# Performance work log

Hardware: AMD Instinct MI355X
Metric: run time of the kernel (lower is better)

## Reference

```python
import jax, jax.numpy as jnp
import numpy as np

M = 64    # multiplicity (channels per harmonic degree)
P = 64    # positional encoding dim
EPS = 1e-5


def sinusoidal_pe(N, P):
    pos = jnp.arange(N, dtype=jnp.float32)[:, None]
    div = jnp.exp(jnp.arange(0, P, 2, dtype=jnp.float32) * (-np.log(10000.0) / P))
    pe = jnp.zeros((N, P), dtype=jnp.float32)
    pe = pe.at[:, 0::2].set(jnp.sin(pos * div))
    pe = pe.at[:, 1::2].set(jnp.cos(pos * div))
    return pe


def split_irreps(h):
    # h: [B, N, 4M] -> scalar part [B,N,M], vector part [B,N,M,3]
    B, N, _ = h.shape
    h4 = h.reshape(B, N, M, 4)
    return h4[..., 0], h4[..., 1:]


def merge_irreps(s, v):
    B, N, _ = s.shape
    return jnp.concatenate([s[..., None], v], axis=-1).reshape(B, N, M * 4)


def hyena_block(h, Wq, Wk, Wv, filt, Wo):
    # Hyena-style gated long convolution: q * conv(k * v), FFT circular conv along seq
    N = h.shape[1]
    q = h @ Wq
    k = h @ Wk
    v = h @ Wv
    kf = jnp.fft.rfft(filt, n=N, axis=0)                       # [N//2+1, H]
    conv = jnp.fft.irfft(jnp.fft.rfft(k * v, n=N, axis=1) * kf[None], n=N, axis=1)
    return (q * conv) @ Wo


def reg_linear(h, W0, W1):
    # degree-wise linear mixing across multiplicity (equivariant)
    s, v = split_irreps(h)
    return merge_irreps(jnp.einsum('bnm,mk->bnk', s, W0),
                        jnp.einsum('bnmd,mk->bnkd', v, W1))


def reg_batchnorm(h, g0, g1):
    # normalize per-channel irrep norms over (batch, tokens); learnable per-channel gain
    s, v = split_irreps(h)
    n0 = jnp.sqrt(jnp.mean(s * s, axis=(0, 1)) + EPS)          # [M]
    n1 = jnp.sqrt(jnp.mean(jnp.sum(v * v, axis=-1), axis=(0, 1)) + EPS)
    return merge_irreps(s / n0 * g0, v / n1[:, None] * g1[:, None])


def norm_activation(h):
    # norm-gated nonlinearity: each irrep scaled by sigmoid of its norm (equivariant)
    s, v = split_irreps(h)
    vn = jnp.sqrt(jnp.sum(v * v, axis=-1, keepdims=True) + EPS)
    return merge_irreps(s * jax.nn.sigmoid(jnp.abs(s)), v * jax.nn.sigmoid(vn))


def setup_inputs() -> dict:
    key = jax.random.key(0)
    B, N = 64, 1024
    D = M * 4
    H = [360, 360, 160]   # 10*sum(2l+1,l<=5)=360, 360, 10*sum(2l+1,l<=3)=160
    ks = iter(jax.random.split(key, 64))
    def rn(shape, scale=0.02):
        return jax.random.normal(next(ks), shape, dtype=jnp.float32) * scale
    inp = {
        'x': jax.random.normal(next(ks), (B, N, 3), dtype=jnp.float32),
        'tok_emb': rn((3, P)),
        'Wf': rn((P, M)),
        'wv': rn((M,), 0.5),
        'w_out': rn((M,), 0.5),
    }
    for i, Hi in enumerate(H, start=1):
        inp[f'Wq{i}'] = rn((D, Hi)); inp[f'Wk{i}'] = rn((D, Hi)); inp[f'Wv{i}'] = rn((D, Hi))
        inp[f'filt{i}'] = rn((N, Hi)); inp[f'Wo{i}'] = rn((Hi, D))
        inp[f'Wm0_{i}'] = rn((M, M)); inp[f'Wm1_{i}'] = rn((M, M))
        inp[f'g0_{i}'] = jnp.ones((M,), jnp.float32); inp[f'g1_{i}'] = jnp.ones((M,), jnp.float32)
    return inp


def reference(x, tok_emb, Wf, wv, w_out,
              Wq1, Wk1, Wv1, filt1, Wo1, Wm0_1, Wm1_1, g0_1, g1_1,
              Wq2, Wk2, Wv2, filt2, Wo2, Wm0_2, Wm1_2, g0_2, g1_2,
              Wq3, Wk3, Wv3, filt3, Wo3, Wm0_3, Wm1_3, g0_3, g1_3):
    B, N, _ = x.shape
    # invariant features: sinusoidal PE + token-type embedding (alternating 0/1, last token 2)
    pe = sinusoidal_pe(N, P)
    tt = jnp.arange(N) % 2
    tt = tt.at[-1].set(2)
    f = pe + tok_emb[tt]                                        # [N, P]
    # input conversion: invariants -> degree-0 channels; input vector -> degree-1 channels
    s0 = jnp.broadcast_to((f @ Wf)[None], (B, N, M))
    v0 = x[:, :, None, :] * wv[None, None, :, None]             # [B, N, M, 3]
    h = merge_irreps(s0, v0)                                    # [B, N, 4M]
    layers = [
        (Wq1, Wk1, Wv1, filt1, Wo1, Wm0_1, Wm1_1, g0_1, g1_1),
        (Wq2, Wk2, Wv2, filt2, Wo2, Wm0_2, Wm1_2, g0_2, g1_2),
        (Wq3, Wk3, Wv3, filt3, Wo3, Wm0_3, Wm1_3, g0_3, g1_3),
    ]
    for (Wq, Wk, Wv_, filt, Wo, Wm0, Wm1, g0, g1) in layers:
        h = h + hyena_block(h, Wq, Wk, Wv_, filt, Wo)           # hyena + residual
        y = reg_linear(h, Wm0, Wm1)                             # mlp
        y = reg_batchnorm(y, g0, g1)                            # batch norm
        y = norm_activation(y)                                  # norm activation
        h = h + y                                               # residual
    pooled = h.mean(axis=1)                                     # [B, 4M] mean pool over tokens
    _, vpool = split_irreps(pooled[:, None, :])                 # [B, 1, M, 3]
    return jnp.einsum('bmd,m->bd', vpool[:, 0], w_out)          # [B, 3]
```

## Files before the change

### kernel.cpp

```cpp
#include <hip/hip_runtime.h>
#include <math.h>

namespace {

typedef __bf16 bf16_t;
typedef bf16_t bf16x8 __attribute__((ext_vector_type(8)));
typedef float floatx4 __attribute__((ext_vector_type(4)));

constexpr int kN = 1024;
constexpr int kM = 64;
constexpr int kP = 64;
constexpr float kEps = 1e-5f;
constexpr int kFN = 1024;
constexpr size_t kYOFF = 16777216;

__device__ __forceinline__ float sigmoidf(float v) { return 1.0f / (1.0f + expf(-v)); }

__device__ __forceinline__ floatx4 mfma16(bf16x8 a, bf16x8 b, floatx4 c) {
  return __builtin_amdgcn_mfma_f32_16x16x32_bf16(a, b, c, 0, 0, 0);
}

__device__ __forceinline__ void fma3(floatx4& acc, bf16x8 ah, bf16x8 al,
                                     bf16x8 bh, bf16x8 bl) {
  acc = mfma16(ah, bh, acc);
  acc = mfma16(ah, bl, acc);
  acc = mfma16(al, bh, acc);
}

__device__ __forceinline__ void fma2(floatx4& acc, bf16x8 ah, bf16x8 bh, bf16x8 bl) {
  acc = mfma16(ah, bh, acc);
  acc = mfma16(ah, bl, acc);
}

union U4 { uint4 u; bf16_t b[8]; };
union Pk4 { uint2 u; bf16_t b[4]; };
union Ub2 { uint u; bf16_t b[2]; };

__device__ __forceinline__ void glds16(const bf16_t* g, bf16_t* l) {
  __builtin_amdgcn_global_load_lds(
      (const __attribute__((address_space(1))) void*)g,
      (__attribute__((address_space(3))) void*)l, 16, 0, 0);
}

__device__ __forceinline__ size_t hidx(int r, int d8) {
  const int rb = r >> 6, rr = r & 63;
  return (size_t)(rb * 8 + (d8 >> 2)) * 4096 + (rr >> 4) * 1024 + (d8 & 3) * 128 + (rr & 15) * 8;
}

__device__ __forceinline__ int zi(int i) { return i + (i >> 4); }

__device__ __forceinline__ float2 cadd(float2 a, float2 b) { return {a.x + b.x, a.y + b.y}; }
__device__ __forceinline__ float2 csub(float2 a, float2 b) { return {a.x - b.x, a.y - b.y}; }
__device__ __forceinline__ float2 cmul(float2 a, float2 w) {
  return {a.x * w.x - a.y * w.y, a.x * w.y + a.y * w.x};
}
__device__ __forceinline__ float2 cmulc(float2 a, float2 w) {
  return {a.x * w.x + a.y * w.y, a.y * w.x - a.x * w.y};
}

__global__ void k_s0(const float* __restrict__ tok_emb, const float* __restrict__ Wf,
                     float* __restrict__ s0) {
  __shared__ float f[kP];
  const int n = blockIdx.x;
  const int t = threadIdx.x;
  const int tt = (n == kN - 1) ? 2 : (n & 1);
  const int j = t >> 1;
  const float cexp = (float)(-9.210340371976184 / 64.0);
  const float divj = expf((float)(2 * j) * cexp);
  const float ang = (float)n * divj;
  const float pe = (t & 1) ? cosf(ang) : sinf(ang);
  f[t] = pe + tok_emb[tt * kP + t];
  __syncthreads();
  float acc = 0.0f;
#pragma unroll 8
  for (int p = 0; p < kP; ++p) acc = fmaf(f[p], Wf[p * kM + t], acc);
  s0[n * kM + t] = acc;
}

__global__ void k_h0(const float* __restrict__ x, const float* __restrict__ wv,
                     const float* __restrict__ s0, bf16_t* __restrict__ hsh) {
  const int idx = blockIdx.x * 256 + threadIdx.x;
  const int r = idx >> 5, d8 = idx & 31;
  const int n = r & (kN - 1);
  const int m0 = d8 * 2, m1 = m0 + 1;
  const float w0 = wv[m0], w1 = wv[m1];
  const float x0 = x[r * 3 + 0], x1 = x[r * 3 + 1], x2 = x[r * 3 + 2];
  float f[8];
  f[0] = s0[n * kM + m0]; f[1] = x0 * w0; f[2] = x1 * w0; f[3] = x2 * w0;
  f[4] = s0[n * kM + m1]; f[5] = x0 * w1; f[6] = x1 * w1; f[7] = x2 * w1;
  U4 oh, ol;
#pragma unroll
  for (int i = 0; i < 8; ++i) {
    const bf16_t h_ = (bf16_t)f[i];
    oh.b[i] = h_; ol.b[i] = (bf16_t)(f[i] - (float)h_);
  }
  const size_t base = hidx(r, d8);
  *(uint4*)(hsh + base) = oh.u;
  *(uint4*)(hsh + base + 512) = ol.u;
}

__global__ void k_wqkv3(const float* __restrict__ Wq0, const float* __restrict__ Wk0,
                        const float* __restrict__ Wv0,
                        const float* __restrict__ Wq1, const float* __restrict__ Wk1,
                        const float* __restrict__ Wv1,
                        const float* __restrict__ Wq2, const float* __restrict__ Wk2,
                        const float* __restrict__ Wv2, bf16_t* __restrict__ wall3) {
  const int l = blockIdx.y;
  const int H = (l == 2) ? 160 : 360;
  const int gy = (l == 2) ? 3 : 6;
  const int c = blockIdx.x;
  if (c >= gy * 64) return;
  const int k = threadIdx.x;
  const float* Wq = (l == 0) ? Wq0 : ((l == 1) ? Wq1 : Wq2);
  const float* Wk = (l == 0) ? Wk0 : ((l == 1) ? Wk1 : Wk2);
  const float* Wv = (l == 0) ? Wv0 : ((l == 1) ? Wv1 : Wv2);
  bf16_t* wall = wall3 + ((l == 2) ? 1179648 : (size_t)l * 589824);
  const bool ok = c < H;
  const float w[3] = {ok ? Wq[k * H + c] : 0.f, ok ? Wk[k * H + c] : 0.f,
                      ok ? Wv[k * H + c] : 0.f};
  const int ct = c >> 6, cgrp = (c >> 4) & 3, cl = c & 15;
  const int kc = k >> 5, quad = (k >> 3) & 3, off = k & 7;
  const size_t base = (size_t)(ct * 8 + kc) * 12288 + cgrp * 512 + quad * 128 + cl * 8 + off;
#pragma unroll
  for (int mat = 0; mat < 3; ++mat) {
    const bf16_t hi = (bf16_t)w[mat];
    wall[base + mat * 4096] = hi;
    wall[base + mat * 4096 + 2048] = (bf16_t)(w[mat] - (float)hi);
  }
}

__global__ void k_wo3(const float* __restrict__ Wo0, const float* __restrict__ Wo1,
                      const float* __restrict__ Wo2, bf16_t* __restrict__ WoF3) {
  const int l = blockIdx.y;
  const int H = (l == 2) ? 160 : 360;
  const float* Wo = (l == 0) ? Wo0 : ((l == 1) ? Wo1 : Wo2);
  bf16_t* WoF = WoF3 + (size_t)l * 196608;
  const int d = blockIdx.x;
  const int c = threadIdx.x;
  const float w = (c < H) ? Wo[c * 256 + d] : 0.f;
  const int dt = d >> 6, dgrp = (d >> 4) & 3, dl = d & 15;
  const int kc = c >> 5, quad = (c >> 3) & 3, off = c & 7;
  const size_t base = (size_t)(dt * 12 + kc) * 4096 + dgrp * 512 + quad * 128 + dl * 8 + off;
  const bf16_t hi = (bf16_t)w;
  WoF[base] = hi;
  WoF[base + 2048] = (bf16_t)(w - (float)hi);
}

__global__ void k_bt3(const float* __restrict__ W00, const float* __restrict__ W10,
                      const float* __restrict__ W01, const float* __restrict__ W11,
                      const float* __restrict__ W02, const float* __restrict__ W12,
                      bf16_t* __restrict__ BtF3) {
  const int l = blockIdx.y;
  const float* W0 = (l == 0) ? W00 : ((l == 1) ? W01 : W02);
  const float* W1 = (l == 0) ? W10 : ((l == 1) ? W11 : W12);
  bf16_t* BtF = BtF3 + (size_t)l * 131072;
  const int col = blockIdx.x, row = threadIdx.x;
  const int k = col >> 2, ck = col & 3, m = row >> 2, cm = row & 3;
  float v = 0.f;
  if (cm == ck) v = (ck == 0 ? W0 : W1)[m * 64 + k];
  const int ct = col >> 6, cgrp = (col >> 4) & 3, cl = col & 15;
  const int kc = row >> 5, quad = (row >> 3) & 3, off = row & 7;
  const size_t base = (size_t)(ct * 8 + kc) * 4096 + cgrp * 512 + quad * 128 + cl * 8 + off;
  const bf16_t hi = (bf16_t)v;
  BtF[base] = hi;
  BtF[base + 2048] = (bf16_t)(v - (float)hi);
}

__global__ void k_tw(float2* __restrict__ twg) {
  const int j = blockIdx.x * 256 + threadIdx.x;
  if (j < kFN / 2) {
    float s, c;
    sincosf(-6.283185307179586f * (float)j / (float)kFN, &s, &c);
    twg[j].x = c; twg[j].y = s;
  }
}

__device__ __forceinline__ void dif_step(float2* z, const float2* tw, int m, int p) {
  const int pm = p & (m - 1);
  const int j = ((p & ~(m - 1)) << 2) | pm;
  const int tm2 = 512 / (2 * m), tm1 = 512 / m;
  const float2 x0 = z[zi(j)], x1 = z[zi(j + m)];
  const float2 x2 = z[zi(j + 2 * m)], x3 = z[zi(j + 3 * m)];
  const float2 w2 = tw[pm * tm2], w2b = tw[(pm + m) * tm2], w1 = tw[pm * tm1];
  const float2 a0 = cadd(x0, x2), a2 = cmul(csub(x0, x2), w2);
  const float2 a1 = cadd(x1, x3), a3 = cmul(csub(x1, x3), w2b);
  z[zi(j)]         = cadd(a0, a1);
  z[zi(j + m)]     = cmul(csub(a0, a1), w1);
  z[zi(j + 2 * m)] = cadd(a2, a3);
  z[zi(j + 3 * m)] = cmul(csub(a2, a3), w1);
}

__device__ __forceinline__ void dit_step(float2* z, const float2* tw, int m, int p) {
  const int pm = p & (m - 1);
  const int j = ((p & ~(m - 1)) << 2) | pm;
  const int tm2 = 512 / (2 * m), tm1 = 512 / m;
  const float2 x0 = z[zi(j)], x1 = z[zi(j + m)];
  const float2 x2 = z[zi(j + 2 * m)], x3 = z[zi(j + 3 * m)];
  const float2 w1 = tw[pm * tm1], w2 = tw[pm * tm2], w2b = tw[(pm + m) * tm2];
  const float2 c1 = cmulc(x1, w1), c3 = cmulc(x3, w1);
  const float2 b0 = cadd(x0, c1), b1 = csub(x0, c1);
  const float2 b2 = cadd(x2, c3), b3 = csub(x2, c3);
  const float2 d2 = cmulc(b2, w2), d3 = cmulc(b3, w2b);
  z[zi(j)]         = cadd(b0, d2);
  z[zi(j + 2 * m)] = csub(b0, d2);
  z[zi(j + m)]     = cadd(b1, d3);
  z[zi(j + 3 * m)] = csub(b1, d3);
}

__device__ void fft_dif(float2* z, const float2* tw) {
  const int p = threadIdx.x;
#pragma unroll
  for (int m = 256; m >= 1; m >>= 2) {
    __syncthreads();
    dif_step(z, tw, m, p);
  }
}

__device__ void fft_dif2_hi(float2* za, float2* zb, const float2* tw) {
  const int p = threadIdx.x;
#pragma unroll
  for (int m = 256; m >= 4; m >>= 2) {
    __syncthreads();
    dif_step(za, tw, m, p);
    dif_step(zb, tw, m, p);
  }
}

__device__ void fft_dit_inv2_hi(float2* za, float2* zb, const float2* tw) {
  const int p = threadIdx.x;
#pragma unroll
  for (int m = 4; m <= 256; m <<= 2) {
    __syncthreads();
    dit_step(za, tw, m, p);
    dit_step(zb, tw, m, p);
  }
}

__global__ __launch_bounds__(256) void k_kf3(const float* __restrict__ f0,
    const float* __restrict__ f1, const float* __restrict__ f2,
    const float2* __restrict__ twg, float2* __restrict__ kf3) {
  __shared__ float2 z[kFN + kFN / 16];
  __shared__ float2 tw[kFN / 2];
  const int bid = blockIdx.x;
  const int l = (bid < 360) ? 0 : ((bid < 720) ? 1 : 2);
  const int c = bid - ((l == 0) ? 0 : ((l == 1) ? 360 : 720));
  const int H = (l == 2) ? 160 : 360;
  const float* filt = (l == 0) ? f0 : ((l == 1) ? f1 : f2);
  float2* kf = kf3 + (size_t)l * 368640;
  for (int j = threadIdx.x; j < kFN / 2; j += 256) tw[j] = twg[j];
  for (int n = threadIdx.x; n < kFN; n += 256) {
    z[zi(n)].x = filt[n * H + c];
    z[zi(n)].y = 0.0f;
  }
  fft_dif(z, tw);
  __syncthreads();
  for (int j = threadIdx.x; j < kFN; j += 256) kf[c * kFN + j] = z[zi(j)];
}

__global__ __launch_bounds__(256) void k_conv(const bf16_t* __restrict__ kvb,
    const bf16_t* __restrict__ qb, bf16_t* __restrict__ prodb,
    const float2* __restrict__ kf, const float2* __restrict__ twg, int H) {
  __shared__ float2 za[kFN + kFN / 16];
  __shared__ float2 zb[kFN + kFN / 16];
  __shared__ float2 tw[kFN / 2];
  const int blk = blockIdx.x;
  const int c = blk % H;
  const int pb = blk / H;
  const size_t off0 = ((size_t)((4 * pb) * H + c)) << 10;
  const size_t off1 = ((size_t)((4 * pb + 1) * H + c)) << 10;
  const size_t off2 = ((size_t)((4 * pb + 2) * H + c)) << 10;
  const size_t off3 = ((size_t)((4 * pb + 3) * H + c)) << 10;
  for (int j = threadIdx.x; j < kFN / 2; j += 256) tw[j] = twg[j];
  for (int n2 = threadIdx.x; n2 < 512; n2 += 256) {
    Ub2 a0, a1, a2, a3;
    a0.u = *(const uint*)(kvb + off0 + 2 * n2);
    a1.u = *(const uint*)(kvb + off1 + 2 * n2);
    a2.u = *(const uint*)(kvb + off2 + 2 * n2);
    a3.u = *(const uint*)(kvb + off3 + 2 * n2);
    za[zi(2 * n2)].x = (float)a0.b[0];     za[zi(2 * n2)].y = (float)a1.b[0];
    za[zi(2 * n2 + 1)].x = (float)a0.b[1]; za[zi(2 * n2 + 1)].y = (float)a1.b[1];
    zb[zi(2 * n2)].x = (float)a2.b[0];     zb[zi(2 * n2)].y = (float)a3.b[0];
    zb[zi(2 * n2 + 1)].x = (float)a2.b[1]; zb[zi(2 * n2 + 1)].y = (float)a3.b[1];
  }
  fft_dif2_hi(za, zb, tw);
  __syncthreads();
  {
    const int p = threadIdx.x;
    const float2 B0 = kf[c * kFN + 4 * p + 0];
    const float2 B1 = kf[c * kFN + 4 * p + 1];
    const float2 B2 = kf[c * kFN + 4 * p + 2];
    const float2 B3 = kf[c * kFN + 4 * p + 3];
#pragma unroll
    for (int arr = 0; arr < 2; ++arr) {
      float2* z = arr ? zb : za;
      const float2 x0 = z[zi(4 * p)], x1 = z[zi(4 * p + 1)];
      const float2 x2 = z[zi(4 * p + 2)], x3 = z[zi(4 * p + 3)];
      const float2 a0 = cadd(x0, x2), a2 = csub(x0, x2);
      const float2 a1 = cadd(x1, x3), dd = csub(x1, x3);
      const float2 a3 = {dd.y, -dd.x};
      const float2 y0 = cadd(a0, a1), y1 = csub(a0, a1);
      const float2 y2 = cadd(a2, a3), y3 = csub(a2, a3);
      const float2 o0 = cmul(y0, B0), o1 = cmul(y1, B1);
      const float2 o2 = cmul(y2, B2), o3 = cmul(y3, B3);
      const float2 t0 = cadd(o0, o1), t1 = csub(o0, o1);
      const float2 t2 = cadd(o2, o3), t3 = csub(o2, o3);
      const float2 d3 = {-t3.y, t3.x};
      z[zi(4 * p)]     = cadd(t0, t2);
      z[zi(4 * p + 2)] = csub(t0, t2);
      z[zi(4 * p + 1)] = cadd(t1, d3);
      z[zi(4 * p + 3)] = csub(t1, d3);
    }
  }
  fft_dit_inv2_hi(za, zb, tw);
  __syncthreads();
  const float s = 1.0f / (float)kFN;
  for (int n2 = threadIdx.x; n2 < 512; n2 += 256) {
    Ub2 q0, q1, q2, q3, o0, o1, o2, o3;
    q0.u = *(const uint*)(qb + off0 + 2 * n2);
    q1.u = *(const uint*)(qb + off1 + 2 * n2);
    q2.u = *(const uint*)(qb + off2 + 2 * n2);
    q3.u = *(const uint*)(qb + off3 + 2 * n2);
    o0.b[0] = (bf16_t)((za[zi(2 * n2)].x * s) * (float)q0.b[0]);
    o0.b[1] = (bf16_t)((za[zi(2 * n2 + 1)].x * s) * (float)q0.b[1]);
    o1.b[0] = (bf16_t)((za[zi(2 * n2)].y * s) * (float)q1.b[0]);
    o1.b[1] = (bf16_t)((za[zi(2 * n2 + 1)].y * s) * (float)q1.b[1]);
    o2.b[0] = (bf16_t)((zb[zi(2 * n2)].x * s) * (float)q2.b[0]);
    o2.b[1] = (bf16_t)((zb[zi(2 * n2 + 1)].x * s) * (float)q2.b[1]);
    o3.b[0] = (bf16_t)((zb[zi(2 * n2)].y * s) * (float)q3.b[0]);
    o3.b[1] = (bf16_t)((zb[zi(2 * n2 + 1)].y * s) * (float)q3.b[1]);
    *(uint*)(prodb + off0 + 2 * n2) = o0.u;
    *(uint*)(prodb + off1 + 2 * n2) = o1.u;
    *(uint*)(prodb + off2 + 2 * n2) = o2.u;
    *(uint*)(prodb + off3 + 2 * n2) = o3.u;
  }
}

__global__ __launch_bounds__(256) void k_qkv(const bf16_t* __restrict__ hsh,
    const bf16_t* __restrict__ wall, int H,
    bf16_t* __restrict__ qtb, bf16_t* __restrict__ kvb) {
  __shared__ bf16_t lds[20480];
  const int gy = (H + 63) >> 6;
  const int bid = blockIdx.x;
  const int xcd = bid & 7, sseq = bid >> 3;
  const int ct = sseq % gy;
  const int rb2 = (sseq / gy) * 8 + xcd;
  const int rb0 = rb2 * 2, rb1 = rb0 + 1;
  const int t = threadIdx.x;
  const int lane = t & 63, wave = t >> 6;
  const int l15 = lane & 15, quad = lane >> 4;
  const int c0 = ct * 64;
  const int wr = (wave & 1) * 32, wc = (wave >> 1) * 32;
  const int wr16 = (wave & 1) * 2, wc16 = (wave >> 1) * 2;
  const int q128l = quad * 128 + l15 * 8;
  floatx4 aq[2][2][2] = {}, ak_[2][2][2] = {}, av_[2][2][2] = {};
  for (int kt = 0; kt < 8; ++kt) {
    {
      const bf16_t* A0 = hsh + (size_t)(rb0 * 8 + kt) * 4096;
      const bf16_t* A1 = hsh + (size_t)(rb1 * 8 + kt) * 4096;
      const bf16_t* Bs = wall + (size_t)(ct * 8 + kt) * 12288;
#pragma unroll
      for (int s = 0; s < 10; ++s) {
        const int seg = wave * 10 + s;
        const bf16_t* src = (seg < 8) ? (A0 + seg * 512)
                          : (seg < 16) ? (A1 + (seg - 8) * 512)
                                       : (Bs + (seg - 16) * 512);
        glds16(src + lane * 8, &lds[seg * 512]);
      }
    }
    __syncthreads();
    bf16x8 ah[2][2], al[2][2];
#pragma unroll
    for (int rbx = 0; rbx < 2; ++rbx)
#pragma unroll
      for (int i = 0; i < 2; ++i) {
        ah[rbx][i] = *(const bf16x8*)(lds + rbx * 4096 + ((wr16 + i) * 2 + 0) * 512 + q128l);
        al[rbx][i] = *(const bf16x8*)(lds + rbx * 4096 + ((wr16 + i) * 2 + 1) * 512 + q128l);
      }
#pragma unroll
    for (int mat = 0; mat < 3; ++mat) {
      const int bb = 8192 + mat * 4096;
#pragma unroll
      for (int j = 0; j < 2; ++j) {
        const bf16x8 bh = *(const bf16x8*)(lds + bb + (wc16 + j) * 512 + q128l);
        const bf16x8 bl = *(const bf16x8*)(lds + bb + 2048 + (wc16 + j) * 512 + q128l);
#pragma unroll
        for (int rbx = 0; rbx < 2; ++rbx)
#pragma unroll
          for (int i = 0; i < 2; ++i) {
            floatx4& a = (mat == 0) ? aq[rbx][i][j]
                       : (mat == 1) ? ak_[rbx][i][j] : av_[rbx][i][j];
            fma3(a, ah[rbx][i], al[rbx][i], bh, bl);
          }
      }
    }
    __syncthreads();
  }
#pragma unroll
  for (int rbx = 0; rbx < 2; ++rbx) {
    const int r0 = (rb0 + rbx) * 64;
    const int b = r0 >> 10;
    const int n0 = r0 & 1023;
#pragma unroll
    for (int j = 0; j < 2; ++j) {
      const int c = c0 + wc + j * 16 + l15;
      if (c < H) {
        const size_t rbw = (((size_t)(b * H + c)) << 10) + n0 + wr + quad * 4;
#pragma unroll
        for (int i = 0; i < 2; ++i) {
          Pk4 pq, pk;
#pragma unroll
          for (int r = 0; r < 4; ++r) {
            pq.b[r] = (bf16_t)aq[rbx][i][j][r];
            pk.b[r] = (bf16_t)(ak_[rbx][i][j][r] * av_[rbx][i][j][r]);
          }
          *(uint2*)(qtb + rbw + i * 16) = pq.u;
          *(uint2*)(kvb + rbw + i * 16) = pk.u;
        }
      }
    }
  }
}

__global__ __launch_bounds__(256) void k_mix(const bf16_t* __restrict__ pv, int H, int KT,
    const bf16_t* __restrict__ WoF, bf16_t* __restrict__ hsh) {
  __shared__ float smem[4352];
  bf16_t* lsm = (bf16_t*)smem;
  const int r0 = blockIdx.x * 64;
  const int t = threadIdx.x;
  const int lane = t & 63, wave = t >> 6;
  const int l15 = lane & 15, quad = lane >> 4;
  const int b = r0 >> 10, n0 = r0 & 1023;
  const int wr = (wave & 1) * 32, wh = wave >> 1;
  const int q128l = quad * 128 + l15 * 8;
  floatx4 acc[2][8] = {};
  const int cl = t >> 3, n8 = (t & 7) * 8;
  {
    U4 val;
    val.u = make_uint4(0, 0, 0, 0);
    if (cl < H)
      val.u = *(const uint4*)(pv + ((((size_t)(b * H + cl)) << 10) + n0 + n8));
#pragma unroll
    for (int u = 0; u < 8; ++u) lsm[(n8 + u) * 40 + cl] = val.b[u];
  }
  for (int kt = 0; kt < KT; ++kt) {
    const int cur = kt & 1;
    const bool have = (kt + 1 < KT);
    U4 nxt;
    nxt.u = make_uint4(0, 0, 0, 0);
    if (have) {
      const int c = (kt + 1) * 32 + cl;
      if (c < H)
        nxt.u = *(const uint4*)(pv + ((((size_t)(b * H + c)) << 10) + n0 + n8));
    }
    __syncthreads();
    const bf16_t* Ls = lsm + cur * 2560;
    const bf16x8 ah0 = *(const bf16x8*)(Ls + (wr + l15) * 40 + quad * 8);
    const bf16x8 ah1 = *(const bf16x8*)(Ls + (wr + 16 + l15) * 40 + quad * 8);
#pragma unroll
    for (int j = 0; j < 8; ++j) {
      const int jj = wh * 8 + j;
      const int dt = jj >> 2, dgrp = jj & 3;
      const bf16_t* Bb = WoF + (size_t)(dt * 12 + kt) * 4096 + dgrp * 512 + q128l;
      const bf16x8 bh = *(const bf16x8*)Bb;
      const bf16x8 bl = *(const bf16x8*)(Bb + 2048);
      fma2(acc[0][j], ah0, bh, bl);
      fma2(acc[1][j], ah1, bh, bl);
    }
    if (have) {
      bf16_t* Ld = lsm + (cur ^ 1) * 2560;
#pragma unroll
      for (int u = 0; u < 8; ++u) Ld[(n8 + u) * 40 + cl] = nxt.b[u];
    }
  }
  const int nl = t >> 2, q4 = t & 3;
  const int r = r0 + nl;
#pragma unroll
  for (int g = 0; g < 4; ++g) {
    __syncthreads();
    if (wh == (g >> 1)) {
#pragma unroll
      for (int jl = 0; jl < 4; ++jl) {
        const int j = (g & 1) * 4 + jl;
#pragma unroll
        for (int i = 0; i < 2; ++i)
#pragma unroll
          for (int rr = 0; rr < 4; ++rr)
            smem[(wr + i * 16 + quad * 4 + rr) * 68 + jl * 16 + l15] = acc[i][j][rr];
      }
    }
    __syncthreads();
#pragma unroll
    for (int u8 = 0; u8 < 2; ++u8) {
      const int d8 = g * 8 + q4 * 2 + u8;
      const size_t base = hidx(r, d8);
      U4 hi, lo;
      hi.u = *(const uint4*)(hsh + base);
      lo.u = *(const uint4*)(hsh + base + 512);
      U4 oh, ol;
#pragma unroll
      for (int i = 0; i < 8; ++i) {
        const float f = (float)hi.b[i] + (float)lo.b[i] +
                        smem[nl * 68 + (q4 * 2 + u8) * 8 + i];
        const bf16_t h_ = (bf16_t)f;
        oh.b[i] = h_; ol.b[i] = (bf16_t)(f - (float)h_);
      }
      *(uint4*)(hsh + base) = oh.u;
      *(uint4*)(hsh + base + 512) = ol.u;
    }
  }
}

__global__ __launch_bounds__(256) void k_reg(const bf16_t* __restrict__ hsh,
    const bf16_t* __restrict__ BtF,
    bf16_t* __restrict__ ybf, float* __restrict__ partial) {
  __shared__ float smf[12288];
  __shared__ float red[256];
  bf16_t* lds = (bf16_t*)smf;
  const int bid = blockIdx.x;
  const int xcd = bid & 7, sseq = bid >> 3;
  const int ct = sseq & 3;
  const int rb2 = (sseq >> 2) * 8 + xcd;
  const int rb0 = rb2 * 2, rb1 = rb0 + 1;
  const int t = threadIdx.x;
  const int lane = t & 63, wave = t >> 6;
  const int l15 = lane & 15, quad = lane >> 4;
  const int c0 = ct * 64;
  const int wr = (wave & 1) * 32, wc = (wave >> 1) * 32;
  const int wr16 = (wave & 1) * 2, wc16 = (wave >> 1) * 2;
  const int q128l = quad * 128 + l15 * 8;
  floatx4 acc[2][2][2] = {};
  auto stage = [&](int kt, int buf) {
    const bf16_t* A0 = hsh + (size_t)(rb0 * 8 + kt) * 4096;
    const bf16_t* A1 = hsh + (size_t)(rb1 * 8 + kt) * 4096;
    const bf16_t* Bs = BtF + (size_t)(ct * 8 + kt) * 4096;
#pragma unroll
    for (int s = 0; s < 6; ++s) {
      const int seg = wave * 6 + s;
      const bf16_t* src = (seg < 8) ? (A0 + seg * 512)
                        : (seg < 16) ? (A1 + (seg - 8) * 512)
                                     : (Bs + (seg - 16) * 512);
      glds16(src + lane * 8, &lds[buf * 12288 + seg * 512]);
    }
  };
  stage(0, 0);
  __syncthreads();
  for (int kt = 0; kt < 8; ++kt) {
    const int cur = kt & 1;
    if (kt < 7) stage(kt + 1, cur ^ 1);
    const bf16_t* Lb = lds + cur * 12288;
    bf16x8 ah[2][2], al[2][2];
#pragma unroll
    for (int rbx = 0; rbx < 2; ++rbx)
#pragma unroll
      for (int i = 0; i < 2; ++i) {
        ah[rbx][i] = *(const bf16x8*)(Lb + rbx * 4096 + ((wr16 + i) * 2 + 0) * 512 + q128l);
        al[rbx][i] = *(const bf16x8*)(Lb + rbx * 4096 + ((wr16 + i) * 2 + 1) * 512 + q128l);
      }
#pragma unroll
    for (int j = 0; j < 2; ++j) {
      const bf16x8 bh = *(const bf16x8*)(Lb + 8192 + (wc16 + j) * 512 + q128l);
      const bf16x8 bl = *(const bf16x8*)(Lb + 8192 + 2048 + (wc16 + j) * 512 + q128l);
#pragma unroll
      for (int rbx = 0; rbx < 2; ++rbx)
#pragma unroll
        for (int i = 0; i < 2; ++i)
          fma3(acc[rbx][i][j], ah[rbx][i], al[rbx][i], bh, bl);
    }
    __syncthreads();
  }
#pragma unroll
  for (int rbx = 0; rbx < 2; ++rbx)
#pragma unroll
    for (int j = 0; j < 2; ++j) {
      float s = 0.f;
#pragma unroll
      for (int i = 0; i < 2; ++i)
#pragma unroll
        for (int r = 0; r < 4; ++r)
          s = fmaf(acc[rbx][i][j][r], acc[rbx][i][j][r], s);
      s += __shfl_down(s, 32);
      s += __shfl_down(s, 16);
      if (lane < 16) red[rbx * 128 + wave * 32 + j * 16 + lane] = s;
    }
#pragma unroll
  for (int rbx = 0; rbx < 2; ++rbx) {
    __syncthreads();
#pragma unroll
    for (int i = 0; i < 2; ++i)
#pragma unroll
      for (int j = 0; j < 2; ++j)
#pragma unroll
        for (int r = 0; r < 4; ++r)
          smf[(wr + i * 16 + quad * 4 + r) * 68 + wc + j * 16 + l15] = acc[rbx][i][j][r];
    __syncthreads();
    const int nl = t >> 2, q4 = t & 3;
    const int r0 = (rb0 + rbx) * 64;
    const size_t gi = (size_t)(r0 + nl) * 256 + c0 + q4 * 16;
#pragma unroll
    for (int u2 = 0; u2 < 2; ++u2) {
      U4 oh, ol;
#pragma unroll
      for (int i = 0; i < 8; ++i) {
        const float f = smf[nl * 68 + q4 * 16 + u2 * 8 + i];
        const bf16_t h_ = (bf16_t)f;
        oh.b[i] = h_; ol.b[i] = (bf16_t)(f - (float)h_);
      }
      *(uint4*)(ybf + gi + u2 * 8) = oh.u;
      *(uint4*)(ybf + kYOFF + gi + u2 * 8) = ol.u;
    }
  }
  if (t < 64) {
    const int w0 = (t >= 32) ? 2 : 0;
    const float v0 = red[w0 * 32 + (t & 31)] + red[(w0 + 1) * 32 + (t & 31)];
    const float v1 = red[128 + w0 * 32 + (t & 31)] + red[128 + (w0 + 1) * 32 + (t & 31)];
    partial[(size_t)rb0 * 256 + c0 + t] = v0;
    partial[(size_t)rb1 * 256 + c0 + t] = v1;
  }
}

__global__ __launch_bounds__(256) void k_stat(const float* __restrict__ partial,
                                              float* __restrict__ st) {
  __shared__ float sm1[16][16];
  __shared__ float tot[16];
  const int bb = blockIdx.x;
  const int t = threadIdx.x;
  const int col16 = t & 15, rgrp = t >> 4;
  const int c = bb * 16 + col16;
  float s = 0.f;
  for (int r = rgrp; r < 1024; r += 16) s += partial[(size_t)r * 256 + c];
  sm1[rgrp][col16] = s;
  __syncthreads();
  if (t < 16) {
    float v = 0.f;
#pragma unroll
    for (int g = 0; g < 16; ++g) v += sm1[g][t];
    tot[t] = v;
  }
  __syncthreads();
  if (t < 4) {
    const int m = bb * 4 + t;
    st[m] = tot[4 * t];
    st[64 + m] = tot[4 * t + 1] + tot[4 * t + 2] + tot[4 * t + 3];
  }
}

__global__ void k_bnact(const bf16_t* __restrict__ ybf, const float* __restrict__ stats,
    const float* __restrict__ g0, const float* __restrict__ g1, bf16_t* __restrict__ hsh) {
  const int idx = blockIdx.x * 256 + threadIdx.x;
  const int r = idx >> 5, d8 = idx & 31;
  const int m0 = d8 * 2, m1 = m0 + 1;
  const float i00 = g0[m0] / sqrtf(stats[m0] * (1.0f / 65536.0f) + kEps);
  const float i10 = g1[m0] / sqrtf(stats[64 + m0] * (1.0f / 65536.0f) + kEps);
  const float i01 = g0[m1] / sqrtf(stats[m1] * (1.0f / 65536.0f) + kEps);
  const float i11 = g1[m1] / sqrtf(stats[64 + m1] * (1.0f / 65536.0f) + kEps);
  const size_t ye = (size_t)r * 256 + d8 * 8;
  U4 yh, yl;
  yh.u = *(const uint4*)(ybf + ye);
  yl.u = *(const uint4*)(ybf + kYOFF + ye);
  float yv[8];
#pragma unroll
  for (int i = 0; i < 8; ++i) yv[i] = (float)yh.b[i] + (float)yl.b[i];
  float a[8];
  {
    const float s = yv[0] * i00;
    const float vx = yv[1] * i10, vy = yv[2] * i10, vz = yv[3] * i10;
    const float so = s * sigmoidf(fabsf(s));
    const float vn = sqrtf(fmaf(vx, vx, fmaf(vy, vy, vz * vz)) + kEps);
    const float gv = sigmoidf(vn);
    a[0] = so; a[1] = vx * gv; a[2] = vy * gv; a[3] = vz * gv;
  }
  {
    const float s = yv[4] * i01;
    const float vx = yv[5] * i11, vy = yv[6] * i11, vz = yv[7] * i11;
    const float so = s * sigmoidf(fabsf(s));
    const float vn = sqrtf(fmaf(vx, vx, fmaf(vy, vy, vz * vz)) + kEps);
    const float gv = sigmoidf(vn);
    a[4] = so; a[5] = vx * gv; a[6] = vy * gv; a[7] = vz * gv;
  }
  const size_t base = hidx(r, d8);
  U4 hi, lo;
  hi.u = *(const uint4*)(hsh + base);
  lo.u = *(const uint4*)(hsh + base + 512);
  U4 oh, ol;
#pragma unroll
  for (int i = 0; i < 8; ++i) {
    const float f = (float)hi.b[i] + (float)lo.b[i] + a[i];
    const bf16_t h_ = (bf16_t)f;
    oh.b[i] = h_; ol.b[i] = (bf16_t)(f - (float)h_);
  }
  *(uint4*)(hsh + base) = oh.u;
  *(uint4*)(hsh + base + 512) = ol.u;
}

__global__ __launch_bounds__(256) void k_pool(const bf16_t* __restrict__ hsh,
    const float* __restrict__ w_out, float* __restrict__ out) {
  __shared__ float r0s[256], r1s[256], r2s[256];
  const int b = blockIdx.x;
  const int t = threadIdx.x;
  float p0 = 0, p1 = 0, p2 = 0;
  for (int idx = t; idx < kN * 32; idx += 256) {
    const int n = idx >> 5, d8 = idx & 31;
    const int r = (b << 10) + n;
    const size_t base = hidx(r, d8);
    U4 hi, lo;
    hi.u = *(const uint4*)(hsh + base);
    lo.u = *(const uint4*)(hsh + base + 512);
    const float w0 = w_out[d8 * 2], w1 = w_out[d8 * 2 + 1];
    p0 += ((float)hi.b[1] + (float)lo.b[1]) * w0 + ((float)hi.b[5] + (float)lo.b[5]) * w1;
    p1 += ((float)hi.b[2] + (float)lo.b[2]) * w0 + ((float)hi.b[6] + (float)lo.b[6]) * w1;
    p2 += ((float)hi.b[3] + (float)lo.b[3]) * w0 + ((float)hi.b[7] + (float)lo.b[7]) * w1;
  }
  r0s[t] = p0; r1s[t] = p1; r2s[t] = p2;
  __syncthreads();
  for (int s = 128; s > 0; s >>= 1) {
    if (t < s) { r0s[t] += r0s[t + s]; r1s[t] += r1s[t + s]; r2s[t] += r2s[t + s]; }
    __syncthreads();
  }
  if (t == 0) {
    out[b * 3 + 0] = r0s[0] * (1.0f / kN);
    out[b * 3 + 1] = r1s[0] * (1.0f / kN);
    out[b * 3 + 2] = r2s[0] * (1.0f / kN);
  }
}

}

extern "C" void kernel_launch(void* const* d_in, const int* in_sizes, int n_in,
                              void* d_out, int out_size, void* d_ws, size_t ws_size,
                              hipStream_t stream) {
  const float* x       = (const float*)d_in[0];
  const float* tok_emb = (const float*)d_in[1];
  const float* Wf      = (const float*)d_in[2];
  const float* wv      = (const float*)d_in[3];
  const float* w_out   = (const float*)d_in[4];

  float* ws    = (float*)d_ws;
  bf16_t* hsh  = (bf16_t*)ws;
  bf16_t* kvb  = (bf16_t*)(ws + 16777216);
  bf16_t* qtb  = (bf16_t*)(ws + 28573696);
  bf16_t* prodb = (bf16_t*)(ws + 40370176);
  bf16_t* ybf  = prodb;
  float*  partial = ws + 40370176 + 20000000;
  float*  s0   = ws + 40370176 + 23592960;
  float*  kf3  = s0 + 65536;
  bf16_t* wall3 = (bf16_t*)(kf3 + 1802240);
  bf16_t* WoF3  = wall3 + 1474560;
  bf16_t* BtF3  = WoF3 + 589824;
  float* stats = (float*)(BtF3 + 393216);
  float* twg   = stats + 384;

  k_tw<<<2, 256, 0, stream>>>((float2*)twg);
  k_s0<<<kN, 64, 0, stream>>>(tok_emb, Wf, s0);
  k_h0<<<8192, 256, 0, stream>>>(x, wv, s0, hsh);
  k_wqkv3<<<dim3(384, 3), 256, 0, stream>>>(
      (const float*)d_in[5], (const float*)d_in[6], (const float*)d_in[7],
      (const float*)d_in[14], (const float*)d_in[15], (const float*)d_in[16],
      (const float*)d_in[23], (const float*)d_in[24], (const float*)d_in[25], wall3);
  k_wo3<<<dim3(256, 3), 384, 0, stream>>>(
      (const float*)d_in[9], (const float*)d_in[18], (const float*)d_in[27], WoF3);
  k_bt3<<<dim3(256, 3), 256, 0, stream>>>(
      (const float*)d_in[10], (const float*)d_in[11],
      (const float*)d_in[19], (const float*)d_in[20],
      (const float*)d_in[28], (const float*)d_in[29], BtF3);
  k_kf3<<<880, 256, 0, stream>>>(
      (const float*)d_in[8], (const float*)d_in[17], (const float*)d_in[26],
      (const float2*)twg, (float2*)kf3);

  for (int l = 0; l < 3; ++l) {
    const float* g0   = (const float*)d_in[5 + 9 * l + 7];
    const float* g1   = (const float*)d_in[5 + 9 * l + 8];
    const int H = (l == 2) ? 160 : 360;
    const int gy = (H + 63) / 64;
    const int KT = gy * 2;
    bf16_t* wall = wall3 + ((l == 2) ? 1179648 : (size_t)l * 589824);
    bf16_t* WoF  = WoF3 + (size_t)l * 196608;
    bf16_t* BtF  = BtF3 + (size_t)l * 131072;
    const float2* kf = (const float2*)kf3 + (size_t)l * 368640;
    float* st = stats + l * 128;

    k_qkv<<<gy * 512, 256, 0, stream>>>(hsh, wall, H, qtb, kvb);
    k_conv<<<16 * H, 256, 0, stream>>>(kvb, qtb, prodb, kf, (const float2*)twg, H);
    k_mix<<<1024, 256, 0, stream>>>(prodb, H, KT, WoF, hsh);
    k_reg<<<2048, 256, 0, stream>>>(hsh, BtF, ybf, partial);
    k_stat<<<16, 256, 0, stream>>>(partial, st);
    k_bnact<<<8192, 256, 0, stream>>>(ybf, st, g0, g1, hsh);
  }

  k_pool<<<64, 256, 0, stream>>>(hsh, w_out, (float*)d_out);
}
```

Before: 1.120 ms.

## Fuse first FFT stage into load, atomic batchnorm stats, split pooling across blocks

The conv kernel now performs the first radix-4 DIF stage in registers right after loading k*v, which removes one shared-memory pass and one barrier. The separate k_stat kernel is dropped: k_reg atomically accumulates per-channel sums into stats that k_qkv zeroes. The final pooling is split across 512 blocks with a tiny second reduction kernel so more of the GPU is occupied. In exchange, atomics make the batchnorm statistic order nondeterministic, and the new load path uses scalar bf16 loads instead of paired uint loads.

```diff
diff --git a/kernel.cpp b/kernel.cpp
--- a/kernel.cpp
+++ b/kernel.cpp
@@ -219,7 +219,7 @@
 __device__ void fft_dif2_hi(float2* za, float2* zb, const float2* tw) {
   const int p = threadIdx.x;
 #pragma unroll
-  for (int m = 256; m >= 4; m >>= 2) {
+  for (int m = 64; m >= 4; m >>= 2) {
     __syncthreads();
     dif_step(za, tw, m, p);
     dif_step(zb, tw, m, p);
@@ -271,16 +271,27 @@
   const size_t off2 = ((size_t)((4 * pb + 2) * H + c)) << 10;
   const size_t off3 = ((size_t)((4 * pb + 3) * H + c)) << 10;
   for (int j = threadIdx.x; j < kFN / 2; j += 256) tw[j] = twg[j];
-  for (int n2 = threadIdx.x; n2 < 512; n2 += 256) {
-    Ub2 a0, a1, a2, a3;
-    a0.u = *(const uint*)(kvb + off0 + 2 * n2);
-    a1.u = *(const uint*)(kvb + off1 + 2 * n2);
-    a2.u = *(const uint*)(kvb + off2 + 2 * n2);
-    a3.u = *(const uint*)(kvb + off3 + 2 * n2);
-    za[zi(2 * n2)].x = (float)a0.b[0];     za[zi(2 * n2)].y = (float)a1.b[0];
-    za[zi(2 * n2 + 1)].x = (float)a0.b[1]; za[zi(2 * n2 + 1)].y = (float)a1.b[1];
-    zb[zi(2 * n2)].x = (float)a2.b[0];     zb[zi(2 * n2)].y = (float)a3.b[0];
-    zb[zi(2 * n2 + 1)].x = (float)a2.b[1]; zb[zi(2 * n2 + 1)].y = (float)a3.b[1];
+  {
+    const int p = threadIdx.x;
+    float2 xa[4], xb[4];
+#pragma unroll
+    for (int e = 0; e < 4; ++e) {
+      const int idx = p + e * 256;
+      xa[e].x = (float)kvb[off0 + idx]; xa[e].y = (float)kvb[off1 + idx];
+      xb[e].x = (float)kvb[off2 + idx]; xb[e].y = (float)kvb[off3 + idx];
+    }
+    const float2 w2 = twg[p], w2b = twg[p + 256], w1 = twg[2 * p];
+#pragma unroll
+    for (int arr = 0; arr < 2; ++arr) {
+      float2* z = arr ? zb : za;
+      const float2* x = arr ? xb : xa;
+      const float2 a0 = cadd(x[0], x[2]), a2 = cmul(csub(x[0], x[2]), w2);
+      const float2 a1 = cadd(x[1], x[3]), a3 = cmul(csub(x[1], x[3]), w2b);
+      z[zi(p)]       = cadd(a0, a1);
+      z[zi(p + 256)] = cmul(csub(a0, a1), w1);
+      z[zi(p + 512)] = cadd(a2, a3);
+      z[zi(p + 768)] = cmul(csub(a2, a3), w1);
+    }
   }
   fft_dif2_hi(za, zb, tw);
   __syncthreads();
@@ -337,15 +348,16 @@
 
 __global__ __launch_bounds__(256) void k_qkv(const bf16_t* __restrict__ hsh,
     const bf16_t* __restrict__ wall, int H,
-    bf16_t* __restrict__ qtb, bf16_t* __restrict__ kvb) {
+    bf16_t* __restrict__ qtb, bf16_t* __restrict__ kvb, float* __restrict__ st) {
   __shared__ bf16_t lds[20480];
   const int gy = (H + 63) >> 6;
   const int bid = blockIdx.x;
+  const int t = threadIdx.x;
+  if (bid == 0 && t < 128) st[t] = 0.0f;
   const int xcd = bid & 7, sseq = bid >> 3;
   const int ct = sseq % gy;
   const int rb2 = (sseq / gy) * 8 + xcd;
   const int rb0 = rb2 * 2, rb1 = rb0 + 1;
-  const int t = threadIdx.x;
   const int lane = t & 63, wave = t >> 6;
   const int l15 = lane & 15, quad = lane >> 4;
   const int c0 = ct * 64;
@@ -512,7 +524,7 @@
 
 __global__ __launch_bounds__(256) void k_reg(const bf16_t* __restrict__ hsh,
     const bf16_t* __restrict__ BtF,
-    bf16_t* __restrict__ ybf, float* __restrict__ partial) {
+    bf16_t* __restrict__ ybf, float* __restrict__ st) {
   __shared__ float smf[12288];
   __shared__ float red[256];
   bf16_t* lds = (bf16_t*)smf;
@@ -613,34 +625,9 @@
     const int w0 = (t >= 32) ? 2 : 0;
     const float v0 = red[w0 * 32 + (t & 31)] + red[(w0 + 1) * 32 + (t & 31)];
     const float v1 = red[128 + w0 * 32 + (t & 31)] + red[128 + (w0 + 1) * 32 + (t & 31)];
-    partial[(size_t)rb0 * 256 + c0 + t] = v0;
-    partial[(size_t)rb1 * 256 + c0 + t] = v1;
-  }
-}
-
-__global__ __launch_bounds__(256) void k_stat(const float* __restrict__ partial,
-                                              float* __restrict__ st) {
-  __shared__ float sm1[16][16];
-  __shared__ float tot[16];
-  const int bb = blockIdx.x;
-  const int t = threadIdx.x;
-  const int col16 = t & 15, rgrp = t >> 4;
-  const int c = bb * 16 + col16;
-  float s = 0.f;
-  for (int r = rgrp; r < 1024; r += 16) s += partial[(size_t)r * 256 + c];
-  sm1[rgrp][col16] = s;
-  __syncthreads();
-  if (t < 16) {
-    float v = 0.f;
-#pragma unroll
-    for (int g = 0; g < 16; ++g) v += sm1[g][t];
-    tot[t] = v;
-  }
-  __syncthreads();
-  if (t < 4) {
-    const int m = bb * 4 + t;
-    st[m] = tot[4 * t];
-    st[64 + m] = tot[4 * t + 1] + tot[4 * t + 2] + tot[4 * t + 3];
+    const int c = c0 + t;
+    const int m = c >> 2, ck = c & 3;
+    atomicAdd(&st[(ck == 0) ? m : (64 + m)], v0 + v1);
   }
 }
 
@@ -693,12 +680,13 @@
 }
 
 __global__ __launch_bounds__(256) void k_pool(const bf16_t* __restrict__ hsh,
-    const float* __restrict__ w_out, float* __restrict__ out) {
+    const float* __restrict__ w_out, float* __restrict__ pp) {
   __shared__ float r0s[256], r1s[256], r2s[256];
-  const int b = blockIdx.x;
+  const int b = blockIdx.x >> 3;
+  const int sl = blockIdx.x & 7;
   const int t = threadIdx.x;
   float p0 = 0, p1 = 0, p2 = 0;
-  for (int idx = t; idx < kN * 32; idx += 256) {
+  for (int idx = sl * 4096 + t; idx < (sl + 1) * 4096; idx += 256) {
     const int n = idx >> 5, d8 = idx & 31;
     const int r = (b << 10) + n;
     const size_t base = hidx(r, d8);
@@ -717,10 +705,19 @@
     __syncthreads();
   }
   if (t == 0) {
-    out[b * 3 + 0] = r0s[0] * (1.0f / kN);
-    out[b * 3 + 1] = r1s[0] * (1.0f / kN);
-    out[b * 3 + 2] = r2s[0] * (1.0f / kN);
-  }
+    pp[blockIdx.x * 3 + 0] = r0s[0];
+    pp[blockIdx.x * 3 + 1] = r1s[0];
+    pp[blockIdx.x * 3 + 2] = r2s[0];
+  }
+}
+
+__global__ void k_pool2(const float* __restrict__ pp, float* __restrict__ out) {
+  const int t = threadIdx.x;
+  const int b = t / 3, comp = t % 3;
+  float s = 0.f;
+#pragma unroll
+  for (int k = 0; k < 8; ++k) s += pp[(b * 8 + k) * 3 + comp];
+  out[t] = s * (1.0f / kN);
 }
 
 }
@@ -778,13 +775,13 @@
     const float2* kf = (const float2*)kf3 + (size_t)l * 368640;
     float* st = stats + l * 128;
 
-    k_qkv<<<gy * 512, 256, 0, stream>>>(hsh, wall, H, qtb, kvb);
+    k_qkv<<<gy * 512, 256, 0, stream>>>(hsh, wall, H, qtb, kvb, st);
     k_conv<<<16 * H, 256, 0, stream>>>(kvb, qtb, prodb, kf, (const float2*)twg, H);
     k_mix<<<1024, 256, 0, stream>>>(prodb, H, KT, WoF, hsh);
-    k_reg<<<2048, 256, 0, stream>>>(hsh, BtF, ybf, partial);
-    k_stat<<<16, 256, 0, stream>>>(partial, st);
+    k_reg<<<2048, 256, 0, stream>>>(hsh, BtF, ybf, st);
     k_bnact<<<8192, 256, 0, stream>>>(ybf, st, g0, g1, hsh);
   }
 
-  k_pool<<<64, 256, 0, stream>>>(hsh, w_out, (float*)d_out);
-}
+  k_pool<<<512, 256, 0, stream>>>(hsh, w_out, partial);
+  k_pool2<<<1, 192, 0, stream>>>(partial, (float*)d_out);
+}
```

New measurement: 2.119 ms. 89.2% more time.
